# Kernel tuning notes

Measured on AMD Instinct MI355X. Metric: run time of the kernel, lower is better.

The kernel has to match this reference:

```python
import jax, jax.numpy as jnp
import numpy as np

DIM = 1024
NUM_HEADS = 16
HEAD_DIM = DIM // NUM_HEADS
SCALE = DIM ** (-0.5)  # NOTE: original scales by full dim, not head_dim


def setup_inputs() -> dict:
    key = jax.random.key(0)
    ks = jax.random.split(key, 5)
    B, S = 2, 2048
    x = jax.random.normal(ks[0], (B, S, DIM), dtype=jnp.float32)
    w_qkv = jax.random.normal(ks[1], (DIM, 3 * DIM), dtype=jnp.float32) * (DIM ** -0.5)
    b_qkv = jax.random.normal(ks[2], (3 * DIM,), dtype=jnp.float32) * 0.02
    w_proj = jax.random.normal(ks[3], (DIM, DIM), dtype=jnp.float32) * (DIM ** -0.5)
    b_proj = jax.random.normal(ks[4], (DIM,), dtype=jnp.float32) * 0.02
    return {"x": x, "w_qkv": w_qkv, "b_qkv": b_qkv, "w_proj": w_proj, "b_proj": b_proj}


def reference(x, w_qkv, b_qkv, w_proj, b_proj):
    B, S, D = x.shape
    qkv = x @ w_qkv + b_qkv                                  # [B,S,3D]
    qkv = qkv.reshape(B, S, NUM_HEADS, 3 * HEAD_DIM).transpose(0, 2, 1, 3)  # [B,H,S,3hd]
    q, k, v = jnp.split(qkv, 3, axis=-1)                     # each [B,H,S,hd]
    attn = jnp.einsum("bhqd,bhkd->bhqk", q, k) * SCALE       # [B,H,S,S]
    attn = jax.nn.softmax(attn, axis=-1)
    out = jnp.einsum("bhqk,bhkd->bhqd", attn, v)             # [B,H,S,hd]
    out = out.transpose(0, 2, 1, 3).reshape(B, S, D)
    return out @ w_proj + b_proj
```

## Files before the change

### kernel.cpp

```cpp
#include <hip/hip_runtime.h>
#include <hip/hip_bf16.h>

#define DIM 1024
#define NH 16
#define HD 64
#define BB 2
#define SS 2048
#define MROWS (BB * SS)
#define SCALE 0.03125f
#define SC_LOG2E 0.04508422002778011f

typedef unsigned short u16;
typedef unsigned int u32;
typedef __attribute__((ext_vector_type(8))) short short8;
typedef __attribute__((ext_vector_type(4))) float f32x4;

#if __has_builtin(__builtin_amdgcn_exp2f)
#define EXP2(x) __builtin_amdgcn_exp2f(x)
#else
#define EXP2(x) __builtin_exp2f(x)
#endif

__device__ __forceinline__ u16 f2bf(float f) {
  union { float f; u32 u; } v; v.f = f;
  return (u16)((v.u + 0x7fffu + ((v.u >> 16) & 1u)) >> 16);
}

__device__ __forceinline__ u32 pack2bf(float a, float b) {
  union { __hip_bfloat162 h; u32 u; } cv;
  cv.h = __float22bfloat162_rn(make_float2(a, b));
  return cv.u;
}

__device__ __forceinline__ void async16(const u16* g, u16* l) {
  __builtin_amdgcn_global_load_lds(
      (const __attribute__((address_space(1))) void*)(const void*)g,
      (__attribute__((address_space(3))) void*)(void*)l, 16, 0, 0);
}

__device__ __forceinline__ short8 ld8(const u16* p) { return *(const short8*)p; }

__global__ void cvt_kernel(const float* __restrict__ in, u16* __restrict__ out, int n4) {
  int i = blockIdx.x * blockDim.x + threadIdx.x;
  if (i < n4) {
    float4 v = ((const float4*)in)[i];
    u32 lo = (u32)f2bf(v.x) | ((u32)f2bf(v.y) << 16);
    u32 hi = (u32)f2bf(v.z) | ((u32)f2bf(v.w) << 16);
    ((uint2*)out)[i] = make_uint2(lo, hi);
  }
}

__global__ void tconv_kernel(const float* __restrict__ in, u16* __restrict__ out, int R, int C) {
  __shared__ u16 t[64 * 65];
  int c0 = blockIdx.x * 64, r0 = blockIdx.y * 64;
  #pragma unroll
  for (int i = 0; i < 16; i++) {
    int j = i * 256 + threadIdx.x;
    int rr = j >> 6, cc = j & 63;
    t[rr * 65 + cc] = f2bf(in[(size_t)(r0 + rr) * C + c0 + cc]);
  }
  __syncthreads();
  #pragma unroll
  for (int i = 0; i < 16; i++) {
    int j = i * 256 + threadIdx.x;
    int oc = j >> 6, orr = j & 63;
    out[(size_t)(c0 + oc) * R + r0 + orr] = t[orr * 65 + oc];
  }
}

template <int MODE>
__global__ __launch_bounds__(256, 2) void gemm_bt(
    const u16* __restrict__ A, const u16* __restrict__ Bt,
    const float* __restrict__ bias, void* __restrict__ C,
    u16* __restrict__ vT, int M, int N, int K) {
  __shared__ __align__(16) u16 As[128 * 32];
  __shared__ __align__(16) u16 Bs[128 * 32];
  const int tid = threadIdx.x;
  const int w = tid >> 6, l = tid & 63;
  const int r = l & 15, q = l >> 4;
  const int m0 = blockIdx.y * 128, n0 = blockIdx.x * 128;
  const int qm = (w & 1) * 64, qn = (w >> 1) * 64;

  const size_t aoff = (size_t)(m0 + w * 16 + (l >> 2)) * K + (size_t)(l & 3) * 8;
  const size_t boff = (size_t)(n0 + w * 16 + (l >> 2)) * K + (size_t)(l & 3) * 8;
  u16* alds = &As[(w * 64 + l) * 8];
  u16* blds = &Bs[(w * 64 + l) * 8];

  f32x4 acc[4][4] = {};
  for (int k0 = 0; k0 < K; k0 += 32) {
    async16(A + aoff + k0, alds);
    async16(A + aoff + (size_t)64 * K + k0, alds + 2048);
    async16(Bt + boff + k0, blds);
    async16(Bt + boff + (size_t)64 * K + k0, blds + 2048);
    __syncthreads();
    short8 af[4], bfr[4];
    #pragma unroll
    for (int i = 0; i < 4; i++) af[i] = ld8(&As[(qm + i * 16 + r) * 32 + q * 8]);
    #pragma unroll
    for (int j = 0; j < 4; j++) bfr[j] = ld8(&Bs[(qn + j * 16 + r) * 32 + q * 8]);
    #pragma unroll
    for (int i = 0; i < 4; i++)
      #pragma unroll
      for (int j = 0; j < 4; j++)
        acc[i][j] = __builtin_amdgcn_mfma_f32_16x16x32_bf16(af[i], bfr[j], acc[i][j], 0, 0, 0);
    __syncthreads();
  }
  #pragma unroll
  for (int i = 0; i < 4; i++) {
    int ro = m0 + qm + i * 16 + q * 4;
    #pragma unroll
    for (int j = 0; j < 4; j++) {
      int col = n0 + qn + j * 16 + r;
      float bv = bias[col];
      float v0 = acc[i][j][0] + bv, v1 = acc[i][j][1] + bv;
      float v2 = acc[i][j][2] + bv, v3 = acc[i][j][3] + bv;
      if (MODE == 1) {
        float* out = (float*)C;
        out[(size_t)(ro + 0) * N + col] = v0;
        out[(size_t)(ro + 1) * N + col] = v1;
        out[(size_t)(ro + 2) * N + col] = v2;
        out[(size_t)(ro + 3) * N + col] = v3;
      } else {
        int h = col / 192, wi = col - h * 192;
        if (wi >= 128) {
          int bb = ro >> 11, s = ro & 2047, d = wi - 128;
          uint2 pk = make_uint2(pack2bf(v0, v1), pack2bf(v2, v3));
          *(uint2*)&vT[((size_t)((bb * NH + h) * HD + d)) * SS + s] = pk;
        } else {
          u16* qk2 = (u16*)C;
          const float sc = (wi < 64) ? SC_LOG2E : 1.0f;
          qk2[(size_t)(ro + 0) * 2048 + h * 128 + wi] = f2bf(v0 * sc);
          qk2[(size_t)(ro + 1) * 2048 + h * 128 + wi] = f2bf(v1 * sc);
          qk2[(size_t)(ro + 2) * 2048 + h * 128 + wi] = f2bf(v2 * sc);
          qk2[(size_t)(ro + 3) * 2048 + h * 128 + wi] = f2bf(v3 * sc);
        }
      }
    }
  }
}

__global__ __launch_bounds__(512, 4) void attn4_kernel(
    const u16* __restrict__ qk2, const u16* __restrict__ vT,
    u16* __restrict__ attno) {
  __shared__ __align__(16) u16 smem[34816];
  u16* Ks = smem;
  u16* Vs = smem + 8192;
  const int tid = threadIdx.x;
  const int w = tid >> 6, l = tid & 63;
  const int r = l & 15, q = l >> 4;
  const int wq = w & 3, ws = w >> 2;
  const int b = blockIdx.z, h = blockIdx.y, q0 = blockIdx.x * 128;

  const u16* qb = qk2 + (size_t)b * SS * 2048;
  const u16* kB = qb + h * 128 + 64;
  const u16* vB = vT + (size_t)((b * NH + h) * HD) * SS;
  u16* pw = smem + 16384 + w * (32 * 72);

  short8 qf[2][2];
  #pragma unroll
  for (int i = 0; i < 2; i++)
    #pragma unroll
    for (int kq = 0; kq < 2; kq++)
      qf[i][kq] = ld8(qb + (size_t)(q0 + wq * 32 + i * 16 + r) * 2048 + h * 128 + kq * 32 + q * 8);

  const int klrow = l >> 3;
  const int kchunk = (l & 7) ^ klrow;
  const int vlrow = l >> 4;
  const int vslot = l & 15;

  const short8 vone = {0x3F80, 0x3F80, 0x3F80, 0x3F80, 0x3F80, 0x3F80, 0x3F80, 0x3F80};
  f32x4 oacc[2][4] = {};
  f32x4 den[2] = {};

  for (int kv0 = 0; kv0 < SS; kv0 += 128) {
    #pragma unroll
    for (int t = 0; t < 2; t++) {
      int g = w * 2 + t;
      async16(kB + (size_t)(kv0 + g * 8 + klrow) * 2048 + kchunk * 8, &Ks[g * 512 + l * 8]);
    }
    #pragma unroll
    for (int t = 0; t < 2; t++) {
      int g = w * 2 + t;
      int d = g * 4 + vlrow;
      int c = vslot ^ (d & 15);
      async16(vB + (size_t)d * SS + kv0 + c * 8, &Vs[g * 512 + l * 8]);
    }
    __syncthreads();

    f32x4 sacc[4][2] = {};
    #pragma unroll
    for (int j2 = 0; j2 < 4; j2++) {
      const u16* krow = &Ks[(ws * 64 + j2 * 16 + r) * 64];
      short8 a0 = ld8(krow + ((q ^ (r & 7)) * 8));
      short8 a1 = ld8(krow + (((4 + q) ^ (r & 7)) * 8));
      #pragma unroll
      for (int i = 0; i < 2; i++) {
        sacc[j2][i] = __builtin_amdgcn_mfma_f32_16x16x32_bf16(a0, qf[i][0], sacc[j2][i], 0, 0, 0);
        sacc[j2][i] = __builtin_amdgcn_mfma_f32_16x16x32_bf16(a1, qf[i][1], sacc[j2][i], 0, 0, 0);
      }
    }
    #pragma unroll
    for (int j2 = 0; j2 < 4; j2++)
      #pragma unroll
      for (int i = 0; i < 2; i++) {
        float p0 = EXP2(sacc[j2][i][0]);
        float p1 = EXP2(sacc[j2][i][1]);
        float p2 = EXP2(sacc[j2][i][2]);
        float p3 = EXP2(sacc[j2][i][3]);
        *(uint2*)&pw[(i * 16 + r) * 72 + j2 * 16 + q * 4] =
            make_uint2(pack2bf(p0, p1), pack2bf(p2, p3));
      }
    #pragma unroll
    for (int ks = 0; ks < 2; ks++) {
      short8 pa0 = ld8(&pw[r * 72 + ks * 32 + q * 8]);
      short8 pa1 = ld8(&pw[(16 + r) * 72 + ks * 32 + q * 8]);
      den[0] = __builtin_amdgcn_mfma_f32_16x16x32_bf16(pa0, vone, den[0], 0, 0, 0);
      den[1] = __builtin_amdgcn_mfma_f32_16x16x32_bf16(pa1, vone, den[1], 0, 0, 0);
      #pragma unroll
      for (int dj = 0; dj < 4; dj++) {
        short8 vb = ld8(&Vs[(dj * 16 + r) * 128 + (((ws * 8 + ks * 4 + q) ^ r) * 8)]);
        oacc[0][dj] = __builtin_amdgcn_mfma_f32_16x16x32_bf16(pa0, vb, oacc[0][dj], 0, 0, 0);
        oacc[1][dj] = __builtin_amdgcn_mfma_f32_16x16x32_bf16(pa1, vb, oacc[1][dj], 0, 0, 0);
      }
    }
    __syncthreads();
  }

  float* part = (float*)smem;
  float* dnf  = part + 8 * 32 * 36;
  const int ho = 1 - ws;
  {
    const int wbase = (wq * 2 + ho) * 32;
    #pragma unroll
    for (int i = 0; i < 2; i++) {
      if (ws == 0) {
        *(f32x4*)&part[(wbase + r) * 36 + i * 16 + q * 4]      = oacc[i][2];
        *(f32x4*)&part[(wbase + 16 + r) * 36 + i * 16 + q * 4] = oacc[i][3];
      } else {
        *(f32x4*)&part[(wbase + r) * 36 + i * 16 + q * 4]      = oacc[i][0];
        *(f32x4*)&part[(wbase + 16 + r) * 36 + i * 16 + q * 4] = oacc[i][1];
      }
      if (r == 0)
        *(f32x4*)&dnf[(ws * 4 + wq) * 32 + i * 16 + q * 4] = den[i];
    }
  }
  __syncthreads();
  {
    const int rbase = (wq * 2 + ws) * 32;
    #pragma unroll
    for (int i = 0; i < 2; i++) {
      f32x4 dt = *(f32x4*)&dnf[(ho * 4 + wq) * 32 + i * 16 + q * 4] + den[i];
      f32x4 oa, ob;
      if (ws == 0) { oa = oacc[i][0]; ob = oacc[i][1]; }
      else         { oa = oacc[i][2]; ob = oacc[i][3]; }
      oa += *(f32x4*)&part[(rbase + r) * 36 + i * 16 + q * 4];
      ob += *(f32x4*)&part[(rbase + 16 + r) * 36 + i * 16 + q * 4];
      #pragma unroll
      for (int e = 0; e < 4; e++) {
        float di = 1.f / dt[e];
        int row = q0 + wq * 32 + i * 16 + q * 4 + e;
        u16* o = &attno[(size_t)(b * SS + row) * DIM + h * HD + ws * 32 + r];
        o[0]  = f2bf(oa[e] * di);
        o[16] = f2bf(ob[e] * di);
      }
    }
  }
}

extern "C" void kernel_launch(void* const* d_in, const int* in_sizes, int n_in,
                              void* d_out, int out_size, void* d_ws, size_t ws_size,
                              hipStream_t stream) {
  const float* x      = (const float*)d_in[0];
  const float* w_qkv  = (const float*)d_in[1];
  const float* b_qkv  = (const float*)d_in[2];
  const float* w_proj = (const float*)d_in[3];
  const float* b_proj = (const float*)d_in[4];
  float* out = (float*)d_out;
  char* ws = (char*)d_ws;
  u16* xb     = (u16*)(ws);
  u16* wqkvT  = (u16*)(ws + ((size_t)8  << 20));
  u16* wprojT = (u16*)(ws + ((size_t)14 << 20));
  u16* qk2    = (u16*)(ws + ((size_t)16 << 20));
  u16* attno  = (u16*)(ws + ((size_t)32 << 20));
  u16* vT     = (u16*)(ws + ((size_t)40 << 20));

  cvt_kernel<<<4096, 256, 0, stream>>>(x, xb, MROWS * DIM / 4);
  tconv_kernel<<<dim3(48, 16), 256, 0, stream>>>(w_qkv, wqkvT, DIM, 3 * DIM);
  tconv_kernel<<<dim3(16, 16), 256, 0, stream>>>(w_proj, wprojT, DIM, DIM);
  gemm_bt<0><<<dim3(24, 32), 256, 0, stream>>>(xb, wqkvT, b_qkv, qk2, vT, MROWS, 3 * DIM, DIM);
  attn4_kernel<<<dim3(16, NH, BB), 512, 0, stream>>>(qk2, vT, attno);
  gemm_bt<1><<<dim3(8, 32), 256, 0, stream>>>(attno, wprojT, b_proj, out, nullptr, MROWS, DIM, DIM);
}
```

Measured before the change: 196.3 us.

## Double-buffer K/V tiles and keep P in registers via permlane swaps

The attention kernel now prefetches the next K/V tile into a second shared-memory buffer while computing on the current one, dropping the load-then-sync wait at the top of each iteration. The exp'd score tile no longer goes through a per-wave shared-memory scratch. Instead it is repacked in registers with v_permlane32/16 swaps into the MFMA A-operand layout, which removes LDS writes and reads for P. Shared memory use changes slightly, and correctness depends on the permlane mapping matching the old LDS layout.

```diff
diff --git a/kernel.cpp b/kernel.cpp
--- a/kernel.cpp
+++ b/kernel.cpp
@@ -14,6 +14,7 @@
 typedef unsigned int u32;
 typedef __attribute__((ext_vector_type(8))) short short8;
 typedef __attribute__((ext_vector_type(4))) float f32x4;
+typedef __attribute__((ext_vector_type(2))) unsigned int u32x2;
 
 #if __has_builtin(__builtin_amdgcn_exp2f)
 #define EXP2(x) __builtin_amdgcn_exp2f(x)
@@ -30,6 +31,23 @@
   union { __hip_bfloat162 h; u32 u; } cv;
   cv.h = __float22bfloat162_rn(make_float2(a, b));
   return cv.u;
+}
+
+__device__ __forceinline__ void plswap32(u32& a, u32& b) {
+#if __has_builtin(__builtin_amdgcn_permlane32_swap)
+  u32x2 t = __builtin_amdgcn_permlane32_swap(a, b, false, false);
+  a = t[0]; b = t[1];
+#else
+  asm("v_permlane32_swap_b32 %0, %1" : "+v"(a), "+v"(b));
+#endif
+}
+__device__ __forceinline__ void plswap16(u32& a, u32& b) {
+#if __has_builtin(__builtin_amdgcn_permlane16_swap)
+  u32x2 t = __builtin_amdgcn_permlane16_swap(a, b, false, false);
+  a = t[0]; b = t[1];
+#else
+  asm("v_permlane16_swap_b32 %0, %1" : "+v"(a), "+v"(b));
+#endif
 }
 
 __device__ __forceinline__ void async16(const u16* g, u16* l) {
@@ -139,12 +157,10 @@
   }
 }
 
-__global__ __launch_bounds__(512, 4) void attn4_kernel(
+__global__ __launch_bounds__(512, 4) void attn5_kernel(
     const u16* __restrict__ qk2, const u16* __restrict__ vT,
     u16* __restrict__ attno) {
-  __shared__ __align__(16) u16 smem[34816];
-  u16* Ks = smem;
-  u16* Vs = smem + 8192;
+  __shared__ __align__(16) u16 smem[32768];
   const int tid = threadIdx.x;
   const int w = tid >> 6, l = tid & 63;
   const int r = l & 15, q = l >> 4;
@@ -154,7 +170,6 @@
   const u16* qb = qk2 + (size_t)b * SS * 2048;
   const u16* kB = qb + h * 128 + 64;
   const u16* vB = vT + (size_t)((b * NH + h) * HD) * SS;
-  u16* pw = smem + 16384 + w * (32 * 72);
 
   short8 qf[2][2];
   #pragma unroll
@@ -168,24 +183,35 @@
   const int vlrow = l >> 4;
   const int vslot = l & 15;
 
+#define STAGE(KV0, DST) do {                                                     \
+    u16* Kd_ = (DST); u16* Vd_ = Kd_ + 8192;                                     \
+    _Pragma("unroll")                                                            \
+    for (int tt = 0; tt < 2; tt++) {                                             \
+      int g = w * 2 + tt;                                                        \
+      async16(kB + (size_t)((KV0) + g * 8 + klrow) * 2048 + kchunk * 8,          \
+              &Kd_[g * 512 + l * 8]);                                            \
+    }                                                                            \
+    _Pragma("unroll")                                                            \
+    for (int tt = 0; tt < 2; tt++) {                                             \
+      int g = w * 2 + tt;                                                        \
+      int d_ = g * 4 + vlrow;                                                    \
+      int c_ = vslot ^ (d_ & 15);                                                \
+      async16(vB + (size_t)d_ * SS + (KV0) + c_ * 8, &Vd_[g * 512 + l * 8]);     \
+    }                                                                            \
+  } while (0)
+
   const short8 vone = {0x3F80, 0x3F80, 0x3F80, 0x3F80, 0x3F80, 0x3F80, 0x3F80, 0x3F80};
   f32x4 oacc[2][4] = {};
   f32x4 den[2] = {};
 
-  for (int kv0 = 0; kv0 < SS; kv0 += 128) {
-    #pragma unroll
-    for (int t = 0; t < 2; t++) {
-      int g = w * 2 + t;
-      async16(kB + (size_t)(kv0 + g * 8 + klrow) * 2048 + kchunk * 8, &Ks[g * 512 + l * 8]);
-    }
-    #pragma unroll
-    for (int t = 0; t < 2; t++) {
-      int g = w * 2 + t;
-      int d = g * 4 + vlrow;
-      int c = vslot ^ (d & 15);
-      async16(vB + (size_t)d * SS + kv0 + c * 8, &Vs[g * 512 + l * 8]);
-    }
-    __syncthreads();
+  STAGE(0, smem);
+  __syncthreads();
+
+  for (int t = 0; t < 16; ++t) {
+    const int cur = t & 1;
+    u16* Ks = smem + cur * 16384;
+    u16* Vs = Ks + 8192;
+    if (t < 15) STAGE((t + 1) * 128, smem + (cur ^ 1) * 16384);
 
     f32x4 sacc[4][2] = {};
     #pragma unroll
@@ -199,32 +225,38 @@
         sacc[j2][i] = __builtin_amdgcn_mfma_f32_16x16x32_bf16(a1, qf[i][1], sacc[j2][i], 0, 0, 0);
       }
     }
-    #pragma unroll
-    for (int j2 = 0; j2 < 4; j2++)
+    short8 pa[2][2];
+    #pragma unroll
+    for (int ks = 0; ks < 2; ks++)
       #pragma unroll
       for (int i = 0; i < 2; i++) {
-        float p0 = EXP2(sacc[j2][i][0]);
-        float p1 = EXP2(sacc[j2][i][1]);
-        float p2 = EXP2(sacc[j2][i][2]);
-        float p3 = EXP2(sacc[j2][i][3]);
-        *(uint2*)&pw[(i * 16 + r) * 72 + j2 * 16 + q * 4] =
-            make_uint2(pack2bf(p0, p1), pack2bf(p2, p3));
+        f32x4 sa = sacc[ks * 2][i], sb = sacc[ks * 2 + 1][i];
+        u32 A0 = pack2bf(EXP2(sa[0]), EXP2(sa[1]));
+        u32 A1 = pack2bf(EXP2(sa[2]), EXP2(sa[3]));
+        u32 B0 = pack2bf(EXP2(sb[0]), EXP2(sb[1]));
+        u32 B1 = pack2bf(EXP2(sb[2]), EXP2(sb[3]));
+        plswap32(A0, B0);
+        plswap32(A1, B1);
+        plswap16(A0, B0);
+        plswap16(A1, B1);
+        union { short8 s8; u32 u[4]; } pk;
+        pk.u[0] = A0; pk.u[1] = A1; pk.u[2] = B0; pk.u[3] = B1;
+        pa[ks][i] = pk.s8;
       }
     #pragma unroll
     for (int ks = 0; ks < 2; ks++) {
-      short8 pa0 = ld8(&pw[r * 72 + ks * 32 + q * 8]);
-      short8 pa1 = ld8(&pw[(16 + r) * 72 + ks * 32 + q * 8]);
-      den[0] = __builtin_amdgcn_mfma_f32_16x16x32_bf16(pa0, vone, den[0], 0, 0, 0);
-      den[1] = __builtin_amdgcn_mfma_f32_16x16x32_bf16(pa1, vone, den[1], 0, 0, 0);
+      den[0] = __builtin_amdgcn_mfma_f32_16x16x32_bf16(pa[ks][0], vone, den[0], 0, 0, 0);
+      den[1] = __builtin_amdgcn_mfma_f32_16x16x32_bf16(pa[ks][1], vone, den[1], 0, 0, 0);
       #pragma unroll
       for (int dj = 0; dj < 4; dj++) {
         short8 vb = ld8(&Vs[(dj * 16 + r) * 128 + (((ws * 8 + ks * 4 + q) ^ r) * 8)]);
-        oacc[0][dj] = __builtin_amdgcn_mfma_f32_16x16x32_bf16(pa0, vb, oacc[0][dj], 0, 0, 0);
-        oacc[1][dj] = __builtin_amdgcn_mfma_f32_16x16x32_bf16(pa1, vb, oacc[1][dj], 0, 0, 0);
+        oacc[0][dj] = __builtin_amdgcn_mfma_f32_16x16x32_bf16(pa[ks][0], vb, oacc[0][dj], 0, 0, 0);
+        oacc[1][dj] = __builtin_amdgcn_mfma_f32_16x16x32_bf16(pa[ks][1], vb, oacc[1][dj], 0, 0, 0);
       }
     }
     __syncthreads();
   }
+#undef STAGE
 
   float* part = (float*)smem;
   float* dnf  = part + 8 * 32 * 36;
@@ -288,6 +320,6 @@
   tconv_kernel<<<dim3(48, 16), 256, 0, stream>>>(w_qkv, wqkvT, DIM, 3 * DIM);
   tconv_kernel<<<dim3(16, 16), 256, 0, stream>>>(w_proj, wprojT, DIM, DIM);
   gemm_bt<0><<<dim3(24, 32), 256, 0, stream>>>(xb, wqkvT, b_qkv, qk2, vT, MROWS, 3 * DIM, DIM);
-  attn4_kernel<<<dim3(16, NH, BB), 512, 0, stream>>>(qk2, vT, attno);
+  attn5_kernel<<<dim3(16, NH, BB), 512, 0, stream>>>(qk2, vT, attno);
   gemm_bt<1><<<dim3(8, 32), 256, 0, stream>>>(attno, wprojT, b_proj, out, nullptr, MROWS, DIM, DIM);
 }
```

Result: faster. 191.3 us (-2.5%).
